# Performance work log

Measured on AMD Instinct MI355X. Metric: run time of the kernel, lower is better.

The kernel has to match this reference:

```python
import jax, jax.numpy as jnp
import numpy as np

N = 8192
INPUT_DIM = 3000
HIDDEN_DIM = 512
LATENT_DIM = 30
AVG_DEGREE = 32


def setup_inputs() -> dict:
    key = jax.random.key(0)
    k_x, k_g, k_w0, k_v0, k_v1, k_w1 = jax.random.split(key, 6)

    node_features = jax.random.normal(k_x, (N, INPUT_DIM), dtype=jnp.float32)

    # Binary adjacency, avg degree ~AVG_DEGREE, with self-loops so every
    # softmax row has at least one entry (mirrors typical spatial graphs).
    p = AVG_DEGREE / N
    adj = (jax.random.uniform(k_g, (N, N)) < p).astype(jnp.float32)
    idx = jnp.arange(N)
    graph = adj.at[idx, idx].set(1.0)

    def xavier(k, shape):
        fan_in, fan_out = shape
        limit = float(np.sqrt(6.0 / (fan_in + fan_out)))
        return jax.random.uniform(k, shape, jnp.float32, -limit, limit)

    W0 = xavier(k_w0, (INPUT_DIM, HIDDEN_DIM))
    v0 = xavier(k_v0, (HIDDEN_DIM, 1))
    v1 = xavier(k_v1, (HIDDEN_DIM, 1))
    W1 = xavier(k_w1, (HIDDEN_DIM, LATENT_DIM))

    return {"node_features": node_features, "graph": graph,
            "W0": W0, "v0": v0, "v1": v1, "W1": W1}


def _gat_layer(X_in, graph, W, v0, v1):
    # Projection
    X = X_in @ W                                   # [N, D]
    # Rank-1 pairwise scores, masked by adjacency
    f0 = X @ v0                                    # [N, 1]
    f1 = X @ v1                                    # [N, 1]
    E = graph * (f0 + f1.T)                        # [N, N]
    scores = jax.nn.sigmoid(E) - 0.5               # values kept by to_sparse
    mask = graph != 0
    # Masked softmax over dim=1 (torch.sparse.softmax over nnz of each row;
    # rows with no edges stay all-zero after to_dense)
    neg = jnp.finfo(scores.dtype).min
    w = jnp.where(mask, scores, neg)
    m = jnp.max(w, axis=1, keepdims=True)
    e = jnp.where(mask, jnp.exp(w - m), 0.0)
    s = jnp.sum(e, axis=1, keepdims=True)
    alphas = e / jnp.maximum(s, jnp.asarray(1e-30, scores.dtype))
    # Weighted aggregation + ELU
    return jax.nn.elu(alphas @ X)


def reference(node_features, graph, W0, v0, v1, W1):
    Z = _gat_layer(node_features, graph, W0, v0, v1)  # layer 0 (attention)
    Z = Z @ W1                                        # last layer: proj only
    return Z
```

## Files before the change

kernel.cpp:

```cpp
#include <hip/hip_runtime.h>
#include <stdint.h>

#define NN   8192
#define KDIM 3000
#define KP   3072
#define KHALF 1536
#define DDIM 512
#define LDIM 30

typedef __attribute__((ext_vector_type(8))) short short8;
typedef __attribute__((ext_vector_type(4))) float float4v;

__device__ __forceinline__ float bf2f(unsigned short h) {
    union { unsigned int u; float f; } v; v.u = ((unsigned int)h) << 16; return v.f;
}
__device__ __forceinline__ unsigned short f2bf(float f) {
    union { float f; unsigned int u; } v; v.f = f;
    unsigned int r = v.u + 0x7FFF + ((v.u >> 16) & 1);
    return (unsigned short)(r >> 16);
}
__device__ __forceinline__ void gl_lds16(const void* g, void* l) {
    __builtin_amdgcn_global_load_lds(
        (const __attribute__((address_space(1))) unsigned int*)g,
        (__attribute__((address_space(3))) unsigned int*)l, 16, 0, 0);
}

__global__ __launch_bounds__(384) void k_prep(
    const float* __restrict__ A, unsigned short* __restrict__ Abf,
    const float* __restrict__ W0, unsigned short* __restrict__ W0T) {
    int bid = blockIdx.x, t = threadIdx.x;
    if (bid < NN) {
        int k = t * 8;
        uint4 o = {0, 0, 0, 0};
        if (k < KDIM) {
            const float* src = A + (size_t)bid * KDIM + k;
            float4 a = *(const float4*)src;
            float4 b = *(const float4*)(src + 4);
            unsigned short* h = (unsigned short*)&o;
            h[0] = f2bf(a.x); h[1] = f2bf(a.y); h[2] = f2bf(a.z); h[3] = f2bf(a.w);
            h[4] = f2bf(b.x); h[5] = f2bf(b.y); h[6] = f2bf(b.z); h[7] = f2bf(b.w);
        }
        *(uint4*)(Abf + (size_t)bid * KP + k) = o;
    } else {
        __shared__ float tile[32][33];
        int b = bid - NN;
        int k0 = (b % 96) * 32, n0 = (b / 96) * 32;
        int tx = t & 31, ty = (t >> 5) & 7;
        if (t < 256) {
            #pragma unroll
            for (int p = 0; p < 4; p++) {
                int k = k0 + ty + p * 8;
                float val = 0.f;
                if (k < KDIM) val = W0[(size_t)k * DDIM + n0 + tx];
                tile[ty + p * 8][tx] = val;
            }
        }
        __syncthreads();
        if (t < 256) {
            #pragma unroll
            for (int p = 0; p < 4; p++) {
                int k = k0 + tx;
                int n = n0 + ty + p * 8;
                W0T[(size_t)n * KP + k] = f2bf(tile[tx][ty + p * 8]);
            }
        }
    }
}

#define BM 128
#define BN 64

__global__ __launch_bounds__(256) void k_gemm(
    const unsigned short* __restrict__ A,
    const unsigned short* __restrict__ BT,
    float* __restrict__ Xpart)
{
    __shared__ __align__(16) unsigned short As[2][BM][32];
    __shared__ __align__(16) unsigned short Bs[2][BN][32];
    int t = threadIdx.x, w = t >> 6, l = t & 63;
    int m0 = blockIdx.x * BM, n0 = blockIdx.y * BN;
    int z  = blockIdx.z;
    int wm = (w & 1) * 64, wn = (w >> 1) * 32;

    float4v acc[4][2];
    #pragma unroll
    for (int mf = 0; mf < 4; mf++)
        #pragma unroll
        for (int nf = 0; nf < 2; nf++)
            acc[mf][nf] = (float4v){0.f, 0.f, 0.f, 0.f};

    int lr = l >> 2;
    int lk = (l & 3) * 8;
    const unsigned short* Abase = A  + (size_t)m0 * KP;
    const unsigned short* Bbase = BT + (size_t)n0 * KP;
    const int lA = l & 15;
    const int qA = (l >> 4) * 8;
    const int kstart = z * KHALF, kend = kstart + KHALF;

    for (int k0 = kstart; k0 < kend; k0 += 64) {
        if (k0 != kstart) __syncthreads();
        #pragma unroll
        for (int p = 0; p < 4; p++) {
            int q = w * 4 + p, h = q >> 3, rb = q & 7;
            gl_lds16(Abase + (size_t)(rb * 16 + lr) * KP + k0 + h * 32 + lk,
                     &As[h][rb * 16][0]);
        }
        #pragma unroll
        for (int p = 0; p < 2; p++) {
            int q = w * 2 + p, h = q >> 2, rb = q & 3;
            gl_lds16(Bbase + (size_t)(rb * 16 + lr) * KP + k0 + h * 32 + lk,
                     &Bs[h][rb * 16][0]);
        }
        __syncthreads();

        #pragma unroll
        for (int h = 0; h < 2; h++) {
            short8 af[4], bfr[2];
            #pragma unroll
            for (int mf = 0; mf < 4; mf++)
                af[mf] = *(const short8*)&As[h][wm + mf * 16 + lA][qA];
            #pragma unroll
            for (int nf = 0; nf < 2; nf++)
                bfr[nf] = *(const short8*)&Bs[h][wn + nf * 16 + lA][qA];
            #pragma unroll
            for (int mf = 0; mf < 4; mf++)
                #pragma unroll
                for (int nf = 0; nf < 2; nf++)
                    acc[mf][nf] = __builtin_amdgcn_mfma_f32_16x16x32_bf16(
                        af[mf], bfr[nf], acc[mf][nf], 0, 0, 0);
        }
    }

    float* Xp = Xpart + (size_t)z * NN * DDIM;
    int rq = (l >> 4) * 4;
    #pragma unroll
    for (int mf = 0; mf < 4; mf++) {
        #pragma unroll
        for (int nf = 0; nf < 2; nf++) {
            int col = n0 + wn + nf * 16 + lA;
            int row = m0 + wm + mf * 16 + rq;
            #pragma unroll
            for (int r = 0; r < 4; r++)
                Xp[(size_t)(row + r) * DDIM + col] = acc[mf][nf][r];
        }
    }
}

__global__ __launch_bounds__(256) void k_combine(
    const float* __restrict__ X0, const float* __restrict__ X1,
    const float* __restrict__ v0, const float* __restrict__ v1,
    unsigned short* __restrict__ Xbf, float* __restrict__ f0, float* __restrict__ f1)
{
    __shared__ float r0[4], r1[4];
    int i = blockIdx.x, t = threadIdx.x;
    int w = t >> 6, l = t & 63;
    size_t base = (size_t)i * DDIM + t * 2;
    float2 xa = *(const float2*)(X0 + base);
    float2 xb = *(const float2*)(X1 + base);
    float x0 = xa.x + xb.x, x1 = xa.y + xb.y;
    unsigned int pack = (unsigned int)f2bf(x0) | ((unsigned int)f2bf(x1) << 16);
    *(unsigned int*)(Xbf + base) = pack;
    float2 va = *(const float2*)(v0 + t * 2);
    float2 vb = *(const float2*)(v1 + t * 2);
    float p0 = x0 * va.x + x1 * va.y;
    float p1 = x0 * vb.x + x1 * vb.y;
    #pragma unroll
    for (int off = 32; off; off >>= 1) {
        p0 += __shfl_down(p0, off);
        p1 += __shfl_down(p1, off);
    }
    if (l == 0) { r0[w] = p0; r1[w] = p1; }
    __syncthreads();
    if (t == 0) f0[i] = r0[0] + r0[1] + r0[2] + r0[3];
    if (t == 1) f1[i] = r1[0] + r1[1] + r1[2] + r1[3];
}

#define CAP 1024
__global__ __launch_bounds__(256) void k_aggregate(
    const float* __restrict__ G,
    const unsigned short* __restrict__ Xbf,
    const float* __restrict__ f0,
    const float* __restrict__ f1,
    const float* __restrict__ W1,
    float* __restrict__ out)
{
    __shared__ int cnt;
    __shared__ int   jlist[CAP];
    __shared__ float elist[CAP];
    __shared__ float zrow[DDIM];
    __shared__ float red[256];
    int t = threadIdx.x;
    int i = blockIdx.x;
    if (t == 0) cnt = 0;
    __syncthreads();

    float f0i = f0[i];
    const float* grow = G + (size_t)i * NN;
    #pragma unroll
    for (int it = 0; it < 8; it++) {
        int base = (it * 256 + t) * 4;
        float4 gv = *(const float4*)(grow + base);
        float g[4] = {gv.x, gv.y, gv.z, gv.w};
        #pragma unroll
        for (int m = 0; m < 4; m++) {
            if (g[m] != 0.f) {
                int j = base + m;
                float xe = f0i + f1[j];
                float sg = 1.0f / (1.0f + __expf(-xe));
                float e  = __expf(sg - 0.5f);
                int p = atomicAdd(&cnt, 1);
                if (p < CAP) { jlist[p] = j; elist[p] = e; }
            }
        }
    }
    __syncthreads();

    int n = cnt < CAP ? cnt : CAP;
    float s = 0.f;
    for (int k = 0; k < n; k++) s += elist[k];
    float inv = 1.0f / fmaxf(s, 1e-30f);

    float a0 = 0.f, a1 = 0.f;
    int k = 0;
    for (; k + 4 <= n; k += 4) {
        int j0 = jlist[k], j1 = jlist[k+1], j2 = jlist[k+2], j3 = jlist[k+3];
        float e0 = elist[k], e1 = elist[k+1], e2 = elist[k+2], e3 = elist[k+3];
        unsigned int x0 = *(const unsigned int*)(Xbf + (size_t)j0 * DDIM + t * 2);
        unsigned int x1 = *(const unsigned int*)(Xbf + (size_t)j1 * DDIM + t * 2);
        unsigned int x2 = *(const unsigned int*)(Xbf + (size_t)j2 * DDIM + t * 2);
        unsigned int x3 = *(const unsigned int*)(Xbf + (size_t)j3 * DDIM + t * 2);
        a0 += e0 * bf2f((unsigned short)(x0 & 0xFFFFu))
            + e1 * bf2f((unsigned short)(x1 & 0xFFFFu))
            + e2 * bf2f((unsigned short)(x2 & 0xFFFFu))
            + e3 * bf2f((unsigned short)(x3 & 0xFFFFu));
        a1 += e0 * bf2f((unsigned short)(x0 >> 16))
            + e1 * bf2f((unsigned short)(x1 >> 16))
            + e2 * bf2f((unsigned short)(x2 >> 16))
            + e3 * bf2f((unsigned short)(x3 >> 16));
    }
    for (; k < n; k++) {
        int j = jlist[k];
        float e = elist[k];
        unsigned int xw = *(const unsigned int*)(Xbf + (size_t)j * DDIM + t * 2);
        a0 += e * bf2f((unsigned short)(xw & 0xFFFFu));
        a1 += e * bf2f((unsigned short)(xw >> 16));
    }
    a0 *= inv; a1 *= inv;
    zrow[2 * t]     = a0 > 0.f ? a0 : __expf(a0) - 1.0f;
    zrow[2 * t + 1] = a1 > 0.f ? a1 : __expf(a1) - 1.0f;
    __syncthreads();

    int c = t & 31, slab = t >> 5;
    float p = 0.f;
    if (c < LDIM) {
        #pragma unroll 4
        for (int q = 0; q < 64; q++) {
            int d = slab * 64 + q;
            p += zrow[d] * W1[d * LDIM + c];
        }
    }
    red[t] = p;
    __syncthreads();
    if (t < LDIM) {
        float sum = 0.f;
        #pragma unroll
        for (int s2 = 0; s2 < 8; s2++) sum += red[s2 * 32 + t];
        out[(size_t)i * LDIM + t] = sum;
    }
}

extern "C" void kernel_launch(void* const* d_in, const int* in_sizes, int n_in,
                              void* d_out, int out_size, void* d_ws, size_t ws_size,
                              hipStream_t stream) {
    (void)in_sizes; (void)n_in; (void)out_size; (void)ws_size;
    const float* nf = (const float*)d_in[0];
    const float* G  = (const float*)d_in[1];
    const float* W0 = (const float*)d_in[2];
    const float* v0 = (const float*)d_in[3];
    const float* v1 = (const float*)d_in[4];
    const float* W1 = (const float*)d_in[5];
    float* out = (float*)d_out;

    char* ws = (char*)d_ws;
    size_t off = 0;
    unsigned short* Abf = (unsigned short*)(ws + off); off += (size_t)NN * KP * 2;
    unsigned short* W0T = (unsigned short*)(ws + off); off += (size_t)DDIM * KP * 2;
    float*          Xp  = (float*)(ws + off);          off += (size_t)2 * NN * DDIM * 4;
    unsigned short* Xbf = (unsigned short*)(ws + off); off += (size_t)NN * DDIM * 2;
    float* f0 = (float*)(ws + off); off += NN * 4;
    float* f1 = (float*)(ws + off); off += NN * 4;

    hipLaunchKernelGGL(k_prep, dim3(NN + 1536), dim3(384), 0, stream, nf, Abf, W0, W0T);
    hipLaunchKernelGGL(k_gemm, dim3(64, 8, 2), dim3(256), 0, stream, Abf, W0T, Xp);
    hipLaunchKernelGGL(k_combine, dim3(NN), dim3(256), 0, stream,
                       Xp, Xp + (size_t)NN * DDIM, v0, v1, Xbf, f0, f1);
    hipLaunchKernelGGL(k_aggregate, dim3(NN), dim3(256), 0, stream, G, Xbf, f0, f1, W1, out);
}
```

Before: 512.3 us.

## Fuse combine into GEMM epilogue, drop split-K, use nontemporal graph loads

Removes the split-K GEMM and its fp32 partial buffers. The bf16 conversion of X and the f0/f1 dot products with v0/v1 now happen in the GEMM epilogue, using shuffle reductions and atomicAdd into f0/f1, which k_prep zeroes with an extra block. This drops the 32MB fp32 partial write and re-read and one kernel launch. The cost is that the GEMM grid halves to 512 blocks, lowering occupancy. The adjacency row loads in aggregate also become nontemporal to avoid polluting the cache.

Result: no change. 508.6 us, median of 2 (-0.7%).

```diff
diff --git a/kernel.cpp b/kernel.cpp
--- a/kernel.cpp
+++ b/kernel.cpp
@@ -4,12 +4,12 @@
 #define NN   8192
 #define KDIM 3000
 #define KP   3072
-#define KHALF 1536
 #define DDIM 512
 #define LDIM 30
 
 typedef __attribute__((ext_vector_type(8))) short short8;
 typedef __attribute__((ext_vector_type(4))) float float4v;
+typedef __attribute__((ext_vector_type(4))) float f4v;
 
 __device__ __forceinline__ float bf2f(unsigned short h) {
     union { unsigned int u; float f; } v; v.u = ((unsigned int)h) << 16; return v.f;
@@ -27,7 +27,8 @@
 
 __global__ __launch_bounds__(384) void k_prep(
     const float* __restrict__ A, unsigned short* __restrict__ Abf,
-    const float* __restrict__ W0, unsigned short* __restrict__ W0T) {
+    const float* __restrict__ W0, unsigned short* __restrict__ W0T,
+    float* __restrict__ f01) {
     int bid = blockIdx.x, t = threadIdx.x;
     if (bid < NN) {
         int k = t * 8;
@@ -41,7 +42,7 @@
             h[4] = f2bf(b.x); h[5] = f2bf(b.y); h[6] = f2bf(b.z); h[7] = f2bf(b.w);
         }
         *(uint4*)(Abf + (size_t)bid * KP + k) = o;
-    } else {
+    } else if (bid < NN + 1536) {
         __shared__ float tile[32][33];
         int b = bid - NN;
         int k0 = (b % 96) * 32, n0 = (b / 96) * 32;
@@ -64,6 +65,9 @@
                 W0T[(size_t)n * KP + k] = f2bf(tile[tx][ty + p * 8]);
             }
         }
+    } else {
+        for (int idx = t; idx < 2 * NN / 4; idx += 384)
+            ((uint4*)f01)[idx] = (uint4){0, 0, 0, 0};
     }
 }
 
@@ -73,13 +77,16 @@
 __global__ __launch_bounds__(256) void k_gemm(
     const unsigned short* __restrict__ A,
     const unsigned short* __restrict__ BT,
-    float* __restrict__ Xpart)
+    const float* __restrict__ v0,
+    const float* __restrict__ v1,
+    unsigned short* __restrict__ Xbf,
+    float* __restrict__ f0,
+    float* __restrict__ f1)
 {
     __shared__ __align__(16) unsigned short As[2][BM][32];
     __shared__ __align__(16) unsigned short Bs[2][BN][32];
     int t = threadIdx.x, w = t >> 6, l = t & 63;
     int m0 = blockIdx.x * BM, n0 = blockIdx.y * BN;
-    int z  = blockIdx.z;
     int wm = (w & 1) * 64, wn = (w >> 1) * 32;
 
     float4v acc[4][2];
@@ -95,10 +102,9 @@
     const unsigned short* Bbase = BT + (size_t)n0 * KP;
     const int lA = l & 15;
     const int qA = (l >> 4) * 8;
-    const int kstart = z * KHALF, kend = kstart + KHALF;
-
-    for (int k0 = kstart; k0 < kend; k0 += 64) {
-        if (k0 != kstart) __syncthreads();
+
+    for (int k0 = 0; k0 < KP; k0 += 64) {
+        if (k0) __syncthreads();
         #pragma unroll
         for (int p = 0; p < 4; p++) {
             int q = w * 4 + p, h = q >> 3, rb = q & 7;
@@ -131,8 +137,9 @@
         }
     }
 
-    float* Xp = Xpart + (size_t)z * NN * DDIM;
     int rq = (l >> 4) * 4;
+    float vc0 = v0[n0 + wn + lA], vc1 = v0[n0 + wn + 16 + lA];
+    float uc0 = v1[n0 + wn + lA], uc1 = v1[n0 + wn + 16 + lA];
     #pragma unroll
     for (int mf = 0; mf < 4; mf++) {
         #pragma unroll
@@ -141,38 +148,24 @@
             int row = m0 + wm + mf * 16 + rq;
             #pragma unroll
             for (int r = 0; r < 4; r++)
-                Xp[(size_t)(row + r) * DDIM + col] = acc[mf][nf][r];
-        }
-    }
-}
-
-__global__ __launch_bounds__(256) void k_combine(
-    const float* __restrict__ X0, const float* __restrict__ X1,
-    const float* __restrict__ v0, const float* __restrict__ v1,
-    unsigned short* __restrict__ Xbf, float* __restrict__ f0, float* __restrict__ f1)
-{
-    __shared__ float r0[4], r1[4];
-    int i = blockIdx.x, t = threadIdx.x;
-    int w = t >> 6, l = t & 63;
-    size_t base = (size_t)i * DDIM + t * 2;
-    float2 xa = *(const float2*)(X0 + base);
-    float2 xb = *(const float2*)(X1 + base);
-    float x0 = xa.x + xb.x, x1 = xa.y + xb.y;
-    unsigned int pack = (unsigned int)f2bf(x0) | ((unsigned int)f2bf(x1) << 16);
-    *(unsigned int*)(Xbf + base) = pack;
-    float2 va = *(const float2*)(v0 + t * 2);
-    float2 vb = *(const float2*)(v1 + t * 2);
-    float p0 = x0 * va.x + x1 * va.y;
-    float p1 = x0 * vb.x + x1 * vb.y;
-    #pragma unroll
-    for (int off = 32; off; off >>= 1) {
-        p0 += __shfl_down(p0, off);
-        p1 += __shfl_down(p1, off);
-    }
-    if (l == 0) { r0[w] = p0; r1[w] = p1; }
-    __syncthreads();
-    if (t == 0) f0[i] = r0[0] + r0[1] + r0[2] + r0[3];
-    if (t == 1) f1[i] = r1[0] + r1[1] + r1[2] + r1[3];
+                Xbf[(size_t)(row + r) * DDIM + col] = f2bf(acc[mf][nf][r]);
+        }
+        #pragma unroll
+        for (int r = 0; r < 4; r++) {
+            float s0 = acc[mf][0][r] * vc0 + acc[mf][1][r] * vc1;
+            float s1 = acc[mf][0][r] * uc0 + acc[mf][1][r] * uc1;
+            #pragma unroll
+            for (int off = 8; off; off >>= 1) {
+                s0 += __shfl_xor(s0, off);
+                s1 += __shfl_xor(s1, off);
+            }
+            if (lA == 0) {
+                int row = m0 + wm + mf * 16 + rq + r;
+                atomicAdd(&f0[row], s0);
+                atomicAdd(&f1[row], s1);
+            }
+        }
+    }
 }
 
 #define CAP 1024
@@ -199,11 +192,10 @@
     #pragma unroll
     for (int it = 0; it < 8; it++) {
         int base = (it * 256 + t) * 4;
-        float4 gv = *(const float4*)(grow + base);
-        float g[4] = {gv.x, gv.y, gv.z, gv.w};
+        f4v gv = __builtin_nontemporal_load((const f4v*)(grow + base));
         #pragma unroll
         for (int m = 0; m < 4; m++) {
-            if (g[m] != 0.f) {
+            if (gv[m] != 0.f) {
                 int j = base + m;
                 float xe = f0i + f1[j];
                 float sg = 1.0f / (1.0f + __expf(-xe));
@@ -285,14 +277,14 @@
     size_t off = 0;
     unsigned short* Abf = (unsigned short*)(ws + off); off += (size_t)NN * KP * 2;
     unsigned short* W0T = (unsigned short*)(ws + off); off += (size_t)DDIM * KP * 2;
-    float*          Xp  = (float*)(ws + off);          off += (size_t)2 * NN * DDIM * 4;
     unsigned short* Xbf = (unsigned short*)(ws + off); off += (size_t)NN * DDIM * 2;
     float* f0 = (float*)(ws + off); off += NN * 4;
     float* f1 = (float*)(ws + off); off += NN * 4;
 
-    hipLaunchKernelGGL(k_prep, dim3(NN + 1536), dim3(384), 0, stream, nf, Abf, W0, W0T);
-    hipLaunchKernelGGL(k_gemm, dim3(64, 8, 2), dim3(256), 0, stream, Abf, W0T, Xp);
-    hipLaunchKernelGGL(k_combine, dim3(NN), dim3(256), 0, stream,
-                       Xp, Xp + (size_t)NN * DDIM, v0, v1, Xbf, f0, f1);
-    hipLaunchKernelGGL(k_aggregate, dim3(NN), dim3(256), 0, stream, G, Xbf, f0, f1, W1, out);
-}
+    hipLaunchKernelGGL(k_prep, dim3(NN + 1536 + 1), dim3(384), 0, stream,
+                       nf, Abf, W0, W0T, f0);
+    hipLaunchKernelGGL(k_gemm, dim3(64, 8), dim3(256), 0, stream,
+                       Abf, W0T, v0, v1, Xbf, f0, f1);
+    hipLaunchKernelGGL(k_aggregate, dim3(NN), dim3(256), 0, stream,
+                       G, Xbf, f0, f1, W1, out);
+}
```
